# Kernel optimization log

Hardware: AMD Instinct MI355X
Metric: run time of the kernel (lower is better)

The kernel has to match this reference:

```python
import jax, jax.numpy as jnp
import numpy as np

B, T, A, H, E = 512, 64, 32, 512, 32


def sinusoidal_pos_encoding(t, dim):
    # t: (B, T) float positions -> (B, T, dim)
    half = dim // 2
    freqs = jnp.exp(-jnp.log(10000.0) * jnp.arange(half, dtype=jnp.float32) / half)
    ang = t[..., None] * freqs  # (B, T, half)
    return jnp.concatenate([jnp.sin(ang), jnp.cos(ang)], axis=-1)


def cat_linear(x, W, b, cat_ids):
    # x: (B, T, Din); W: (E, Din, Dout); b: (E, Dout); cat_ids: (B,)
    Wg = W[cat_ids]            # (B, Din, Dout) gathered per-sample weights
    bg = b[cat_ids][:, None]   # (B, 1, Dout)
    return jnp.einsum('btd,bdh->bth', x, Wg) + bg


def swish(x):
    return x * jax.nn.sigmoid(x)


def setup_inputs() -> dict:
    key = jax.random.key(0)
    ks = jax.random.split(key, 10)
    s = lambda fan_in: 1.0 / np.sqrt(fan_in)
    return {
        'actions': jax.random.normal(ks[0], (B, T, A), dtype=jnp.float32),
        'timesteps': jax.random.uniform(ks[1], (B,), dtype=jnp.float32),
        'cat_ids': jax.random.randint(ks[2], (B,), 0, E),
        'W1': jax.random.normal(ks[3], (E, A, H), dtype=jnp.float32) * s(A),
        'b1': jnp.zeros((E, H), dtype=jnp.float32),
        'W2': jax.random.normal(ks[4], (E, 2 * H, H), dtype=jnp.float32) * s(2 * H),
        'b2': jnp.zeros((E, H), dtype=jnp.float32),
        'W3': jax.random.normal(ks[5], (E, H, H), dtype=jnp.float32) * s(H),
        'b3': jnp.zeros((E, H), dtype=jnp.float32),
    }


def reference(actions, timesteps, cat_ids, W1, b1, W2, b2, W3, b3):
    b, t, _ = actions.shape
    timesteps_bt = jnp.broadcast_to(timesteps[:, None], (b, t))
    a_emb = cat_linear(actions, W1, b1, cat_ids)              # (B, T, H)
    tau_emb = sinusoidal_pos_encoding(timesteps_bt, H).astype(a_emb.dtype)
    x = jnp.concatenate([a_emb, tau_emb], axis=-1)            # (B, T, 2H)
    x = swish(cat_linear(x, W2, b2, cat_ids))                 # (B, T, H)
    x = cat_linear(x, W3, b3, cat_ids)                        # (B, T, H)
    return x
```

## Files before the change

### kernel.cpp

```cpp
#include <hip/hip_runtime.h>
#include <hip/hip_bf16.h>

#define B_ 512
#define T_ 64
#define A_ 32
#define H_ 512
#define E_ 32
#define MAX_TASKS 272
#define CAP_ 168
#define GRID_ (8 * CAP_)
#define TSC 16

typedef unsigned short u16;
typedef unsigned int u32;
typedef __attribute__((ext_vector_type(8))) short short8;
typedef __attribute__((ext_vector_type(4))) float floatx4;

static __device__ __forceinline__ u16 f2bf(float f) {
    u32 u = __builtin_bit_cast(u32, f);
    u += 0x7fffu + ((u >> 16) & 1u);
    return (u16)(u >> 16);
}

static __device__ __forceinline__ void gl2lds16(const u16* g, u16* l) {
    __builtin_amdgcn_global_load_lds(
        (const __attribute__((address_space(1))) void*)g,
        (__attribute__((address_space(3))) void*)l, 16, 0, 0);
}

__global__ __launch_bounds__(512) void embed_group_kernel(
        const float* __restrict__ actions, const float* __restrict__ timesteps,
        const int* __restrict__ cat_ids, const float* __restrict__ W1,
        const float* __restrict__ b1, const float* __restrict__ b2,
        u16* __restrict__ a_emb, float* __restrict__ tauG,
        float* __restrict__ bias2s,
        int* __restrict__ sample_list, int4* __restrict__ tasks,
        int* __restrict__ itemlist, int* __restrict__ eoff_g,
        int* __restrict__ ecnt_g) {
    int tid = threadIdx.x;

    if (blockIdx.x == B_) {
        __shared__ int cnt[E_], off[E_], cur[E_], toff[E_], jc[8];
        __shared__ int total, fb;
        if (tid < E_) { cnt[tid] = 0; cur[tid] = 0; }
        __syncthreads();
        int e = cat_ids[tid];
        atomicAdd(&cnt[e], 1);
        __syncthreads();
        if (tid == 0) {
            int run = 0, trun = 0;
            for (int i = 0; i < E_; i++) {
                off[i] = run;  run += cnt[i];
                toff[i] = trun; trun += (cnt[i] + 1) >> 1;
            }
            total = trun;
        }
        __syncthreads();
        if (tid < E_) {
            int c = cnt[tid], o = off[tid], to = toff[tid];
            eoff_g[tid] = o;
            ecnt_g[tid] = c;
            for (int j = 0; j < c; j += 2)
                tasks[to++] = make_int4(tid, o + j, (c - j >= 2) ? 2 : 1, 0);
        }
        if (tid < 8) {
            int J = 0;
            for (int cc = 0; cc < 4; cc++)
                J += 4 * ((cnt[tid + 8 * cc] + 1) >> 1);
            jc[tid] = J;
        }
        __syncthreads();
        if (tid == 0) {
            int f = 0;
            for (int x = 0; x < 8; x++) if (jc[x] > CAP_) f = 1;
            fb = f;
        }
        __syncthreads();
        if (!fb) {
            if (tid < 8) {
                int j = 0;
                for (int cc = 0; cc < 4; cc++) {
                    int ee = tid + 8 * cc;
                    int nt = (cnt[ee] + 1) >> 1, t0 = toff[ee];
                    for (int t = t0; t < t0 + nt; t++)
                        for (int nb = 0; nb < 4; nb++) {
                            itemlist[tid + 8 * j] = (t << 2) | nb;
                            j++;
                        }
                }
                for (; j < CAP_; j++) itemlist[tid + 8 * j] = -1;
            }
        } else {
            for (int f = tid; f < GRID_; f += 512)
                itemlist[f] = (f < 4 * total) ? f : -1;
        }
        int p = atomicAdd(&cur[e], 1);
        sample_list[off[e] + p] = tid;
        return;
    }

    int b = blockIdx.x;
    int e = cat_ids[b];
    {
        float tval = timesteps[b];
        int kk = tid & 255;
        float freq = expf(-9.210340371976184f * (float)kk * (1.0f / 256.0f));
        float ang = tval * freq;
        tauG[(size_t)b * H_ + tid] = (tid < 256) ? sinf(ang) : cosf(ang);
        bias2s[(size_t)b * H_ + tid] = b2[e * H_ + tid];
    }

    __shared__ float act[T_ * A_];
    const float* asrc = actions + (size_t)b * T_ * A_;
    for (int i = tid; i < T_ * A_; i += 512) act[i] = asrc[i];
    __syncthreads();

    const float* w1 = W1 + (size_t)e * A_ * H_;
    float wcol[A_];
#pragma unroll
    for (int k = 0; k < A_; k++) wcol[k] = w1[k * H_ + tid];
    float bb = b1[e * H_ + tid];
    u16* orow = a_emb + (size_t)b * T_ * H_;
    for (int tt = 0; tt < T_; tt++) {
        float acc = bb;
#pragma unroll
        for (int k = 0; k < A_; k++)
            acc = fmaf(act[tt * A_ + k], wcol[k], acc);
        orow[tt * H_ + tid] = f2bf(acc);
    }
}

static __device__ __forceinline__ void ct_block(
        const float* __restrict__ W, u16* __restrict__ Wt,
        int srcK, int dstK, int e, int k0, int n) {
    const float* src = W + ((size_t)e * srcK + k0) * H_ + n;
    short8 out[8];
#pragma unroll
    for (int j = 0; j < 64; j++)
        out[j >> 3][j & 7] = (short)f2bf(src[(size_t)j * H_]);
    u16* dst = Wt + ((size_t)e * H_ + n) * dstK + k0;
#pragma unroll
    for (int c = 0; c < 8; c++) *(short8*)(dst + c * 8) = out[c];
}

__global__ __launch_bounds__(256) void convert_transpose(
        const float* __restrict__ W, u16* __restrict__ Wt, int srcK, int dstK) {
    ct_block(W, Wt, srcK, dstK, blockIdx.z, blockIdx.x * 64,
             blockIdx.y * 256 + threadIdx.x);
}

__global__ __launch_bounds__(256) void prep_kernel(
        const float* __restrict__ W2, u16* __restrict__ Wt2a,
        const float* __restrict__ tauG, const int* __restrict__ sample_list,
        const int* __restrict__ eoff, const int* __restrict__ ecnt,
        float* __restrict__ bias2s) {
    int tid = threadIdx.x;
    int bid = blockIdx.x;

    if (bid < 512) {
        int e = bid >> 4, sub = bid & 15;
        ct_block(W2, Wt2a, 2 * H_, H_, e, (sub & 7) * 64,
                 (sub >> 3) * 256 + tid);
        return;
    }

    __shared__ float tauT[64][17];
    int id = bid - 512;
    int nh = id & 1;
    int ks = (id >> 1) & 7;
    int e  = id >> 4;
    int cnt = ecnt[e], off = eoff[e];
    if (cnt == 0) return;
    int wv = tid >> 6, ln = tid & 63;
    const float* wb = W2 + ((size_t)e * 1024 + 512 + ks * 64) * H_
                      + nh * 256 + ln * 4;
    float* bout = bias2s + nh * 256 + ln * 4;

    for (int c0 = 0; c0 < cnt; c0 += TSC) {
        for (int i = tid; i < TSC * 64; i += 256) {
            int sl = i >> 6, k = i & 63;
            float v = 0.f;
            if (c0 + sl < cnt)
                v = tauG[(size_t)sample_list[off + c0 + sl] * H_ + ks * 64 + k];
            tauT[k][sl] = v;
        }
        __syncthreads();

        float4 a0 = {0,0,0,0}, a1 = {0,0,0,0}, a2 = {0,0,0,0}, a3 = {0,0,0,0};
#pragma unroll 8
        for (int k = 0; k < 64; k++) {
            float4 w4 = *(const float4*)(wb + (size_t)k * H_);
            float t0 = tauT[k][wv * 4 + 0];
            float t1 = tauT[k][wv * 4 + 1];
            float t2 = tauT[k][wv * 4 + 2];
            float t3 = tauT[k][wv * 4 + 3];
            a0.x = fmaf(t0, w4.x, a0.x); a0.y = fmaf(t0, w4.y, a0.y);
            a0.z = fmaf(t0, w4.z, a0.z); a0.w = fmaf(t0, w4.w, a0.w);
            a1.x = fmaf(t1, w4.x, a1.x); a1.y = fmaf(t1, w4.y, a1.y);
            a1.z = fmaf(t1, w4.z, a1.z); a1.w = fmaf(t1, w4.w, a1.w);
            a2.x = fmaf(t2, w4.x, a2.x); a2.y = fmaf(t2, w4.y, a2.y);
            a2.z = fmaf(t2, w4.z, a2.z); a2.w = fmaf(t2, w4.w, a2.w);
            a3.x = fmaf(t3, w4.x, a3.x); a3.y = fmaf(t3, w4.y, a3.y);
            a3.z = fmaf(t3, w4.z, a3.z); a3.w = fmaf(t3, w4.w, a3.w);
        }

#pragma unroll
        for (int si = 0; si < 4; si++) {
            int sl = wv * 4 + si;
            if (c0 + sl < cnt) {
                int s = sample_list[off + c0 + sl];
                float4 a = (si == 0) ? a0 : (si == 1) ? a1 : (si == 2) ? a2 : a3;
                float* p = bout + (size_t)s * H_;
                unsafeAtomicAdd(p + 0, a.x);
                unsafeAtomicAdd(p + 1, a.y);
                unsafeAtomicAdd(p + 2, a.z);
                unsafeAtomicAdd(p + 3, a.w);
            }
        }
        __syncthreads();
    }
}

template <int DIN, bool PSBIAS, bool DO_SWISH, bool OUT_BF16>
__global__ __launch_bounds__(256, 2) void moe_gemm(
        const u16* __restrict__ xsrc, const u16* __restrict__ Wt,
        const float* __restrict__ bias,
        const int* __restrict__ sample_list, const int4* __restrict__ tasks,
        const int* __restrict__ itemlist, void* __restrict__ outp) {
    int item = itemlist[blockIdx.x];
    if (item < 0) return;
    int4 task = tasks[item >> 2];
    int nb = item & 3;
    int ns = task.z;
    int e = task.x;
    int s0 = sample_list[task.y];
    int s1 = (ns > 1) ? sample_list[task.y + 1] : s0;
    int n0 = nb * 128;

    int tid = threadIdx.x;
    int lane = tid & 63, wv = tid >> 6;
    int wr = wv >> 1, wc = wv & 1;
    int quad = lane >> 4, c15 = lane & 15;
    int r8 = lane >> 3, cg = lane & 7;

    __shared__ __align__(16) u16 xs[2][128 * 64];
    __shared__ __align__(16) u16 wt[2][128 * 64];

    floatx4 acc[4][4];
    floatx4 zero4 = {0.f, 0.f, 0.f, 0.f};
#pragma unroll
    for (int i = 0; i < 4; i++)
#pragma unroll
        for (int j = 0; j < 4; j++) acc[i][j] = zero4;

    const u16* wbase = Wt + (size_t)(e * H_ + n0) * DIN;
    int kc_sw = (cg ^ r8) * 8;

    auto stage = [&](int b, int k0) {
#pragma unroll
        for (int h = 0; h < 4; h++) {
            int rbase = h * 32 + wv * 8;
            int s = (h < 2) ? s0 : s1;
            int t = (rbase + r8) & 63;
            gl2lds16(xsrc + ((size_t)s * T_ + t) * H_ + k0 + kc_sw,
                     &xs[b][rbase * 64]);
        }
#pragma unroll
        for (int h = 0; h < 4; h++) {
            int nbase = h * 32 + wv * 8;
            gl2lds16(wbase + (size_t)(nbase + r8) * DIN + k0 + kc_sw,
                     &wt[b][nbase * 64]);
        }
    };

    auto compute = [&](int b) {
#pragma unroll
        for (int kk = 0; kk < 2; kk++) {
            int c = kk * 4 + quad;
            short8 af[4], bfr[4];
#pragma unroll
            for (int i = 0; i < 4; i++) {
                int row = wr * 64 + i * 16 + c15;
                af[i] = *(const short8*)&xs[b][row * 64 + ((c ^ (row & 7)) * 8)];
                int nr = wc * 64 + i * 16 + c15;
                bfr[i] = *(const short8*)&wt[b][nr * 64 + ((c ^ (nr & 7)) * 8)];
            }
#pragma unroll
            for (int mt = 0; mt < 4; mt++)
#pragma unroll
                for (int nt = 0; nt < 4; nt++)
                    acc[mt][nt] = __builtin_amdgcn_mfma_f32_16x16x32_bf16(
                            af[mt], bfr[nt], acc[mt][nt], 0, 0, 0);
        }
    };

    constexpr int KI = DIN / 64;
    stage(0, 0);
    stage(1, 64);
    asm volatile("s_waitcnt vmcnt(8)" ::: "memory");
    __builtin_amdgcn_s_barrier();
    __builtin_amdgcn_sched_barrier(0);
#pragma unroll
    for (int t = 0; t < KI; ++t) {
        compute(t & 1);
        if (t + 1 < KI) {
            __builtin_amdgcn_s_barrier();
            __builtin_amdgcn_sched_barrier(0);
            if (t + 2 < KI) {
                stage(t & 1, (t + 2) * 64);
                asm volatile("s_waitcnt vmcnt(8)" ::: "memory");
            } else {
                asm volatile("s_waitcnt vmcnt(0)" ::: "memory");
            }
            __builtin_amdgcn_s_barrier();
            __builtin_amdgcn_sched_barrier(0);
        }
    }

    if (wr >= ns) return;
    int s = (wr == 0) ? s0 : s1;
    const float* bp = PSBIAS ? (bias + (size_t)s * H_)
                             : (bias + (size_t)e * H_);
#pragma unroll
    for (int mt = 0; mt < 4; mt++) {
        int tb = mt * 16 + quad * 4;
#pragma unroll
        for (int nt = 0; nt < 4; nt++) {
            int col = n0 + wc * 64 + nt * 16 + c15;
            float bv = bp[col];
#pragma unroll
            for (int r = 0; r < 4; r++) {
                float v = acc[mt][nt][r] + bv;
                if (DO_SWISH) v = v / (1.0f + expf(-v));
                size_t oidx = ((size_t)s * T_ + tb + r) * H_ + col;
                if (OUT_BF16) ((u16*)outp)[oidx] = f2bf(v);
                else          ((float*)outp)[oidx] = v;
            }
        }
    }
}

extern "C" void kernel_launch(void* const* d_in, const int* in_sizes, int n_in,
                              void* d_out, int out_size, void* d_ws, size_t ws_size,
                              hipStream_t stream) {
    const float* actions   = (const float*)d_in[0];
    const float* timesteps = (const float*)d_in[1];
    const int*   cat_ids   = (const int*)d_in[2];
    const float* W1 = (const float*)d_in[3];
    const float* b1 = (const float*)d_in[4];
    const float* W2 = (const float*)d_in[5];
    const float* b2 = (const float*)d_in[6];
    const float* W3 = (const float*)d_in[7];
    const float* b3 = (const float*)d_in[8];

    char* ws = (char*)d_ws;
    u16* a_emb = (u16*)ws;
    u16* y     = (u16*)(ws + (size_t)32 * 1024 * 1024);
    char* meta = ws + (size_t)64 * 1024 * 1024 + 512 * 1024;
    int*  sample_list = (int*)meta;
    int4* tasks       = (int4*)(meta + 8192);
    int*  itemlist    = (int*)(meta + 16384);
    int*  eoff        = (int*)(meta + 24576);
    int*  ecnt        = (int*)(meta + 24576 + 128);
    u16*  Wt2a   = (u16*)d_out;
    float* bias2s = (float*)((char*)d_out + (size_t)48 * 1024 * 1024);
    float* tauG   = (float*)((char*)d_out + (size_t)52 * 1024 * 1024);
    u16*  Wt3    = a_emb;

    hipLaunchKernelGGL(embed_group_kernel, dim3(B_ + 1), dim3(512), 0, stream,
                       actions, timesteps, cat_ids, W1, b1, b2,
                       a_emb, tauG, bias2s,
                       sample_list, tasks, itemlist, eoff, ecnt);
    hipLaunchKernelGGL(prep_kernel, dim3(1024), dim3(256), 0, stream,
                       W2, Wt2a, tauG, sample_list, eoff, ecnt, bias2s);
    hipLaunchKernelGGL((moe_gemm<H_, true, true, true>), dim3(GRID_),
                       dim3(256), 0, stream,
                       a_emb, Wt2a, bias2s, sample_list, tasks, itemlist,
                       (void*)y);
    hipLaunchKernelGGL(convert_transpose, dim3(H_ / 64, 2, E_), dim3(256),
                       0, stream, W3, Wt3, H_, H_);
    hipLaunchKernelGGL((moe_gemm<H_, false, false, false>), dim3(GRID_),
                       dim3(256), 0, stream,
                       y, Wt3, b3, sample_list, tasks, itemlist, d_out);
}
```

Before: 303.3 us.

## Compute tau-bias over full K per block, drop atomics, halve transpose tile

The per-sample bias from the tau embedding times W2's lower half is now computed over the full 512-wide K range inside a single block, one output column per lane. Each result is written directly with b2 added, which removes the split-K float atomic adds and the separate bias initialisation in the embed kernel. The weight convert-transpose blocks now handle 32 rows instead of 64, doubling block count for more parallelism. In exchange, each tau-bias block stages a much larger shared tile (512x20 floats), which lowers occupancy, and runs a longer serial K loop with scalar weight loads instead of float4 loads.

```diff
diff --git a/kernel.cpp b/kernel.cpp
--- a/kernel.cpp
+++ b/kernel.cpp
@@ -9,7 +9,6 @@
 #define MAX_TASKS 272
 #define CAP_ 168
 #define GRID_ (8 * CAP_)
-#define TSC 16
 
 typedef unsigned short u16;
 typedef unsigned int u32;
@@ -31,9 +30,8 @@
 __global__ __launch_bounds__(512) void embed_group_kernel(
         const float* __restrict__ actions, const float* __restrict__ timesteps,
         const int* __restrict__ cat_ids, const float* __restrict__ W1,
-        const float* __restrict__ b1, const float* __restrict__ b2,
+        const float* __restrict__ b1,
         u16* __restrict__ a_emb, float* __restrict__ tauG,
-        float* __restrict__ bias2s,
         int* __restrict__ sample_list, int4* __restrict__ tasks,
         int* __restrict__ itemlist, int* __restrict__ eoff_g,
         int* __restrict__ ecnt_g) {
@@ -107,7 +105,6 @@
         float freq = expf(-9.210340371976184f * (float)kk * (1.0f / 256.0f));
         float ang = tval * freq;
         tauG[(size_t)b * H_ + tid] = (tid < 256) ? sinf(ang) : cosf(ang);
-        bias2s[(size_t)b * H_ + tid] = b2[e * H_ + tid];
     }
 
     __shared__ float act[T_ * A_];
@@ -130,78 +127,72 @@
     }
 }
 
-static __device__ __forceinline__ void ct_block(
+static __device__ __forceinline__ void ct_block32(
         const float* __restrict__ W, u16* __restrict__ Wt,
         int srcK, int dstK, int e, int k0, int n) {
     const float* src = W + ((size_t)e * srcK + k0) * H_ + n;
-    short8 out[8];
-#pragma unroll
-    for (int j = 0; j < 64; j++)
+    short8 out[4];
+#pragma unroll
+    for (int j = 0; j < 32; j++)
         out[j >> 3][j & 7] = (short)f2bf(src[(size_t)j * H_]);
     u16* dst = Wt + ((size_t)e * H_ + n) * dstK + k0;
 #pragma unroll
-    for (int c = 0; c < 8; c++) *(short8*)(dst + c * 8) = out[c];
+    for (int c = 0; c < 4; c++) *(short8*)(dst + c * 8) = out[c];
 }
 
 __global__ __launch_bounds__(256) void convert_transpose(
         const float* __restrict__ W, u16* __restrict__ Wt, int srcK, int dstK) {
-    ct_block(W, Wt, srcK, dstK, blockIdx.z, blockIdx.x * 64,
-             blockIdx.y * 256 + threadIdx.x);
+    ct_block32(W, Wt, srcK, dstK, blockIdx.z, blockIdx.x * 32,
+               blockIdx.y * 256 + threadIdx.x);
 }
 
 __global__ __launch_bounds__(256) void prep_kernel(
         const float* __restrict__ W2, u16* __restrict__ Wt2a,
-        const float* __restrict__ tauG, const int* __restrict__ sample_list,
+        const float* __restrict__ tauG, const float* __restrict__ b2,
+        const int* __restrict__ sample_list,
         const int* __restrict__ eoff, const int* __restrict__ ecnt,
         float* __restrict__ bias2s) {
     int tid = threadIdx.x;
     int bid = blockIdx.x;
 
-    if (bid < 512) {
-        int e = bid >> 4, sub = bid & 15;
-        ct_block(W2, Wt2a, 2 * H_, H_, e, (sub & 7) * 64,
-                 (sub >> 3) * 256 + tid);
+    __shared__ float tauT[512][20];
+
+    if (bid < 1024) {
+        int e = bid >> 5, sub = bid & 31;
+        ct_block32(W2, Wt2a, 2 * H_, H_, e, (sub & 15) * 32,
+                   (sub >> 4) * 256 + tid);
         return;
     }
 
-    __shared__ float tauT[64][17];
-    int id = bid - 512;
-    int nh = id & 1;
-    int ks = (id >> 1) & 7;
-    int e  = id >> 4;
+    int id = bid - 1024;
+    int cc = id & 7;
+    int e  = id >> 3;
     int cnt = ecnt[e], off = eoff[e];
     if (cnt == 0) return;
     int wv = tid >> 6, ln = tid & 63;
-    const float* wb = W2 + ((size_t)e * 1024 + 512 + ks * 64) * H_
-                      + nh * 256 + ln * 4;
-    float* bout = bias2s + nh * 256 + ln * 4;
-
-    for (int c0 = 0; c0 < cnt; c0 += TSC) {
-        for (int i = tid; i < TSC * 64; i += 256) {
-            int sl = i >> 6, k = i & 63;
+    int n = cc * 64 + ln;
+    const float* wb = W2 + ((size_t)e * 1024 + 512) * H_ + n;
+    float bcol = b2[e * H_ + n];
+
+    for (int c0 = 0; c0 < cnt; c0 += 16) {
+        for (int i = tid; i < 16 * 512; i += 256) {
+            int sl = i >> 9, k = i & 511;
             float v = 0.f;
             if (c0 + sl < cnt)
-                v = tauG[(size_t)sample_list[off + c0 + sl] * H_ + ks * 64 + k];
+                v = tauG[(size_t)sample_list[off + c0 + sl] * H_ + k];
             tauT[k][sl] = v;
         }
         __syncthreads();
 
-        float4 a0 = {0,0,0,0}, a1 = {0,0,0,0}, a2 = {0,0,0,0}, a3 = {0,0,0,0};
+        float a0 = 0.f, a1 = 0.f, a2 = 0.f, a3 = 0.f;
 #pragma unroll 8
-        for (int k = 0; k < 64; k++) {
-            float4 w4 = *(const float4*)(wb + (size_t)k * H_);
-            float t0 = tauT[k][wv * 4 + 0];
-            float t1 = tauT[k][wv * 4 + 1];
-            float t2 = tauT[k][wv * 4 + 2];
-            float t3 = tauT[k][wv * 4 + 3];
-            a0.x = fmaf(t0, w4.x, a0.x); a0.y = fmaf(t0, w4.y, a0.y);
-            a0.z = fmaf(t0, w4.z, a0.z); a0.w = fmaf(t0, w4.w, a0.w);
-            a1.x = fmaf(t1, w4.x, a1.x); a1.y = fmaf(t1, w4.y, a1.y);
-            a1.z = fmaf(t1, w4.z, a1.z); a1.w = fmaf(t1, w4.w, a1.w);
-            a2.x = fmaf(t2, w4.x, a2.x); a2.y = fmaf(t2, w4.y, a2.y);
-            a2.z = fmaf(t2, w4.z, a2.z); a2.w = fmaf(t2, w4.w, a2.w);
-            a3.x = fmaf(t3, w4.x, a3.x); a3.y = fmaf(t3, w4.y, a3.y);
-            a3.z = fmaf(t3, w4.z, a3.z); a3.w = fmaf(t3, w4.w, a3.w);
+        for (int k = 0; k < 512; k++) {
+            float w = wb[(size_t)k * H_];
+            float4 t4 = *(const float4*)&tauT[k][wv * 4];
+            a0 = fmaf(t4.x, w, a0);
+            a1 = fmaf(t4.y, w, a1);
+            a2 = fmaf(t4.z, w, a2);
+            a3 = fmaf(t4.w, w, a3);
         }
 
 #pragma unroll
@@ -209,12 +200,8 @@
             int sl = wv * 4 + si;
             if (c0 + sl < cnt) {
                 int s = sample_list[off + c0 + sl];
-                float4 a = (si == 0) ? a0 : (si == 1) ? a1 : (si == 2) ? a2 : a3;
-                float* p = bout + (size_t)s * H_;
-                unsafeAtomicAdd(p + 0, a.x);
-                unsafeAtomicAdd(p + 1, a.y);
-                unsafeAtomicAdd(p + 2, a.z);
-                unsafeAtomicAdd(p + 3, a.w);
+                float av = (si == 0) ? a0 : (si == 1) ? a1 : (si == 2) ? a2 : a3;
+                bias2s[(size_t)s * H_ + n] = av + bcol;
             }
         }
         __syncthreads();
@@ -368,16 +355,16 @@
     u16*  Wt3    = a_emb;
 
     hipLaunchKernelGGL(embed_group_kernel, dim3(B_ + 1), dim3(512), 0, stream,
-                       actions, timesteps, cat_ids, W1, b1, b2,
-                       a_emb, tauG, bias2s,
+                       actions, timesteps, cat_ids, W1, b1,
+                       a_emb, tauG,
                        sample_list, tasks, itemlist, eoff, ecnt);
-    hipLaunchKernelGGL(prep_kernel, dim3(1024), dim3(256), 0, stream,
-                       W2, Wt2a, tauG, sample_list, eoff, ecnt, bias2s);
+    hipLaunchKernelGGL(prep_kernel, dim3(1280), dim3(256), 0, stream,
+                       W2, Wt2a, tauG, b2, sample_list, eoff, ecnt, bias2s);
     hipLaunchKernelGGL((moe_gemm<H_, true, true, true>), dim3(GRID_),
                        dim3(256), 0, stream,
                        a_emb, Wt2a, bias2s, sample_list, tasks, itemlist,
                        (void*)y);
-    hipLaunchKernelGGL(convert_transpose, dim3(H_ / 64, 2, E_), dim3(256),
+    hipLaunchKernelGGL(convert_transpose, dim3(H_ / 32, 2, E_), dim3(256),
                        0, stream, W3, Wt3, H_, H_);
     hipLaunchKernelGGL((moe_gemm<H_, false, false, false>), dim3(GRID_),
                        dim3(256), 0, stream,
```

Result: slower. 349.4 us (+15.2%).
